# Optimization experiments

Hardware: AMD Instinct MI355X
Metric: run time of the kernel (lower is better)

Reference implementation:

```python
import jax, jax.numpy as jnp
import numpy as np

EPS = 1e-6

def _l2norm(t):
    # F.normalize over channel axis (axis=1) of (B, dk, L)
    n = jnp.sqrt(jnp.sum(t * t, axis=1, keepdims=True))
    return t / jnp.maximum(n, EPS)

def setup_inputs() -> dict:
    key = jax.random.key(0)
    ks = jax.random.split(key, 8)
    B, Cin, Cenc, dk, dv, H, W = 2, 64, 96, 64, 64, 96, 96
    return {
        "x": jax.random.normal(ks[0], (B, Cin, H, W), dtype=jnp.float32),
        "x_enc": jax.random.normal(ks[1], (B, Cenc, H, W), dtype=jnp.float32),
        "Wq": jax.random.normal(ks[2], (dk, Cenc), dtype=jnp.float32) * 0.05,
        "bq": jax.random.normal(ks[3], (dk,), dtype=jnp.float32) * 0.05,
        "Wk": jax.random.normal(ks[4], (dk, Cenc), dtype=jnp.float32) * 0.05,
        "bk": jax.random.normal(ks[5], (dk,), dtype=jnp.float32) * 0.05,
        "Wv": jax.random.normal(ks[6], (dv, Cin), dtype=jnp.float32) * 0.05,
        "bv": jax.random.normal(ks[7], (dv,), dtype=jnp.float32) * 0.05,
    }

def reference(x, x_enc, Wq, bq, Wk, bk, Wv, bv):
    B, _, H, W = x.shape
    L = H * W
    # 1x1 conv projections == channel matmuls, then flatten spatial dims
    Q = (jnp.einsum('bchw,kc->bkhw', x_enc, Wq) + bq[None, :, None, None]).reshape(B, -1, L)
    K = (jnp.einsum('bchw,kc->bkhw', x_enc, Wk) + bk[None, :, None, None]).reshape(B, -1, L)
    V = (jnp.einsum('bchw,kc->bkhw', x, Wv) + bv[None, :, None, None]).reshape(B, -1, L)
    # per-position L2 normalization over the dk channel axis ('l2' mode)
    Q = _l2norm(Q)
    K = _l2norm(K)
    # A[b,i,j] = sum_q Q[b,q,i] * K[b,q,j], softmax over j
    A = jax.nn.softmax(jnp.einsum('bqi,bqj->bij', Q, K), axis=-1)  # (B, L, L)
    R = jnp.einsum('bij,bvj->bvi', A, V)  # (B, dv, L)
    return R.reshape(B, -1, H, W)
```

## Files before the change

kernel.cpp:

```cpp
#include <hip/hip_runtime.h>
#include <hip/hip_bf16.h>
#include <math.h>

#define NB   2
#define CIN  64
#define CENC 96
#define DK   64
#define DV   64
#define LL   9216
#define QBLK 128
#define KVBLK 64
#define NQT  (LL/QBLK)
#define LOG2E 1.44269504088896340736f

typedef __attribute__((ext_vector_type(8)))  short short8;
typedef __attribute__((ext_vector_type(16))) float f32x16;
typedef __attribute__((ext_vector_type(2)))  unsigned int uint2v;
typedef unsigned int uint;

__device__ inline void gload16(const void* g, void* l) {
    __builtin_amdgcn_global_load_lds(
        (const __attribute__((address_space(1))) unsigned int*)g,
        (__attribute__((address_space(3))) unsigned int*)l, 16, 0, 0);
}

__device__ inline unsigned short f2bf(float f) {
    union { float f; uint u; } v; v.f = f;
    uint r = (v.u + 0x7FFFu + ((v.u >> 16) & 1u)) >> 16;
    return (unsigned short)r;
}

__device__ inline float bf2f(uint u) {
    union { uint u; float f; } c; c.u = u << 16; return c.f;
}

__device__ inline uint pack_bf16x2(float lo, float hi) {
    __hip_bfloat162 h = __float22bfloat162_rn(float2{lo, hi});
    union { __hip_bfloat162 h; uint u; } cvt; cvt.h = h;
    return cvt.u;
}

__device__ inline void plswap(uint& a, uint& b) {
#if __has_builtin(__builtin_amdgcn_permlane32_swap)
    uint2v r = __builtin_amdgcn_permlane32_swap(a, b, false, false);
    a = r.x; b = r.y;
#else
    const int lane = threadIdx.x & 63;
    uint t = (lane < 32) ? b : a;
    t = __shfl_xor(t, 32, 64);
    uint an = (lane < 32) ? a : t;
    uint bn = (lane < 32) ? t : b;
    a = an; b = bn;
#endif
}

__global__ __launch_bounds__(256) void proj_kernel(
    const float* __restrict__ x, const float* __restrict__ x_enc,
    const float* __restrict__ Wq, const float* __restrict__ bq,
    const float* __restrict__ Wk, const float* __restrict__ bk,
    const float* __restrict__ Wv, const float* __restrict__ bv,
    unsigned short* __restrict__ Qb, unsigned short* __restrict__ Kb,
    unsigned short* __restrict__ Vt, int nqk)
{
    __shared__ float sh[2 * CENC * 64];
    const int tid = threadIdx.x;

    if ((int)blockIdx.x < nqk) {
        float* Wt0 = sh;
        float* Wt1 = sh + CENC * 64;
        for (int idx = tid; idx < DK * CENC; idx += 256) {
            int k = idx / CENC, c = idx - k * CENC;
            Wt0[c * 64 + (k ^ (c & 31))] = Wq[idx];
            Wt1[c * 64 + (k ^ (c & 31))] = Wk[idx];
        }
        __syncthreads();

        const int w    = __builtin_amdgcn_readfirstlane(tid >> 6);
        const int lane = tid & 63;
        const int gw   = blockIdx.x * 4 + w;
        const int p0g  = gw * 16;
        const int b    = p0g / LL;
        const int p0   = p0g - b * LL;

        float qa[16], ka[16];
        const float bqv = bq[lane], bkv = bk[lane];
#pragma unroll
        for (int p = 0; p < 16; ++p) { qa[p] = bqv; ka[p] = bkv; }

        const float* xp = x_enc + (size_t)b * CENC * LL + p0;
#pragma unroll 4
        for (int c = 0; c < CENC; ++c) {
            const float wq = Wt0[c * 64 + (lane ^ (c & 31))];
            const float wk = Wt1[c * 64 + (lane ^ (c & 31))];
            const float* xc = xp + (size_t)c * LL;
#pragma unroll
            for (int p = 0; p < 16; ++p) {
                const float xv = xc[p];
                qa[p] = fmaf(wq, xv, qa[p]);
                ka[p] = fmaf(wk, xv, ka[p]);
            }
        }

        unsigned short* qrow = Qb + (size_t)(b * LL + p0) * 64 + lane;
        unsigned short* krow = Kb + (size_t)(b * LL + p0) * 64 + lane;
#pragma unroll
        for (int p = 0; p < 16; ++p) {
            float sq = qa[p] * qa[p];
            float sk = ka[p] * ka[p];
#pragma unroll
            for (int m = 1; m < 64; m <<= 1) {
                sq += __shfl_xor(sq, m, 64);
                sk += __shfl_xor(sk, m, 64);
            }
            qrow[(size_t)p * 64] = f2bf(qa[p] * (LOG2E / fmaxf(sqrtf(sq), 1e-6f)));
            krow[(size_t)p * 64] = f2bf(ka[p] * (1.f / fmaxf(sqrtf(sk), 1e-6f)));
        }
    } else {
        float* Wt = sh;
        unsigned short* Vsh = (unsigned short*)(sh + CIN * 64);
        for (int idx = tid; idx < DV * CIN; idx += 256) {
            int v = idx / CIN, c = idx - v * CIN;
            Wt[c * 64 + (v ^ (c & 31))] = Wv[idx];
        }
        __syncthreads();

        const int w    = __builtin_amdgcn_readfirstlane(tid >> 6);
        const int lane = tid & 63;
        const int l0g  = ((int)blockIdx.x - nqk) * 64;
        const int b    = l0g / LL;
        const int l0   = l0g - b * LL;
        const int p0   = w * 16;

        float va[16];
        const float bvv = bv[lane];
#pragma unroll
        for (int p = 0; p < 16; ++p) va[p] = bvv;

        const float* xp = x + (size_t)b * CIN * LL + l0 + p0;
#pragma unroll 4
        for (int c = 0; c < CIN; ++c) {
            const float wv = Wt[c * 64 + (lane ^ (c & 31))];
            const float* xc = xp + (size_t)c * LL;
#pragma unroll
            for (int p = 0; p < 16; ++p) va[p] = fmaf(wv, xc[p], va[p]);
        }
#pragma unroll
        for (int p = 0; p < 16; ++p) Vsh[(p0 + p) * 64 + lane] = f2bf(va[p]);
        __syncthreads();

        const int v = tid & 63, w2 = tid >> 6;
        uint pk[8];
#pragma unroll
        for (int j = 0; j < 8; ++j)
            pk[j] = (uint)Vsh[(w2 * 16 + 2 * j) * 64 + v] |
                    ((uint)Vsh[(w2 * 16 + 2 * j + 1) * 64 + v] << 16);
        uint4* dst = (uint4*)(Vt + (size_t)b * 64 * LL + (size_t)v * LL + l0 + w2 * 16);
        dst[0] = make_uint4(pk[0], pk[1], pk[2], pk[3]);
        dst[1] = make_uint4(pk[4], pk[5], pk[6], pk[7]);
    }
}

__global__ __launch_bounds__(256, 4) void flash_kernel(
    const unsigned short* __restrict__ Qb,
    const unsigned short* __restrict__ Kb,
    const unsigned short* __restrict__ Vt,
    float* __restrict__ Sp, unsigned short* __restrict__ Rp,
    int JS, int nt)
{
    __shared__ unsigned short Kl[2][KVBLK * 64];
    __shared__ unsigned short Vl[2][64 * KVBLK];

    const int bid0  = blockIdx.x;
    const int chunk = gridDim.x >> 3;
    const int bid   = (bid0 & 7) * chunk + (bid0 >> 3);

    const int qt  = bid % NQT;
    const int js  = (bid / NQT) % JS;
    const int b   = bid / (NQT * JS);
    const int tid = threadIdx.x;
    const int w = tid >> 6, lane = tid & 63;
    const int ln = lane & 31, h = lane >> 5;
    const int i0w = qt * QBLK + w * 32;

    short8 qf[4];
#pragma unroll
    for (int kc = 0; kc < 4; ++kc)
        qf[kc] = *(const short8*)(Qb + ((size_t)(b * LL + i0w + ln)) * 64 + kc * 16 + h * 8);

    const int o0 = w * 1024 + lane * 16;
    const int o1 = o0 + 4096;
    const int r0 = o0 >> 7, r1 = o1 >> 7;
    const int c0 = ((o0 >> 4) & 7) ^ (r0 & 7);
    const int c1 = ((o1 >> 4) & 7) ^ (r1 & 7);

    const unsigned short* KbB = Kb + (size_t)b * LL * 64;
    const unsigned short* VtB = Vt + (size_t)b * 64 * LL;

    f32x16 racc[2];
#pragma unroll
    for (int vg = 0; vg < 2; ++vg)
#pragma unroll
        for (int r = 0; r < 16; ++r) racc[vg][r] = 0.f;
    float ssum = 0.f;

    int j0 = js * nt * KVBLK;
    gload16(KbB + (size_t)(j0 + r0) * 64 + c0 * 8, (char*)Kl[0] + w * 1024);
    gload16(KbB + (size_t)(j0 + r1) * 64 + c1 * 8, (char*)Kl[0] + w * 1024 + 4096);
    gload16(VtB + (size_t)r0 * LL + j0 + c0 * 8, (char*)Vl[0] + w * 1024);
    gload16(VtB + (size_t)r1 * LL + j0 + c1 * 8, (char*)Vl[0] + w * 1024 + 4096);

    for (int t = 0; t < nt; ++t, j0 += KVBLK) {
        __syncthreads();
        const int bb = t & 1;
        if (t + 1 < nt) {
            const int j1 = j0 + KVBLK;
            gload16(KbB + (size_t)(j1 + r0) * 64 + c0 * 8, (char*)Kl[bb ^ 1] + w * 1024);
            gload16(KbB + (size_t)(j1 + r1) * 64 + c1 * 8, (char*)Kl[bb ^ 1] + w * 1024 + 4096);
            gload16(VtB + (size_t)r0 * LL + j1 + c0 * 8, (char*)Vl[bb ^ 1] + w * 1024);
            gload16(VtB + (size_t)r1 * LL + j1 + c1 * 8, (char*)Vl[bb ^ 1] + w * 1024 + 4096);
        }
        const char* Klb = (const char*)Kl[bb];
        const char* Vlb = (const char*)Vl[bb];

#pragma unroll
        for (int jt = 0; jt < 2; ++jt) {
            f32x16 sacc;
#pragma unroll
            for (int r = 0; r < 16; ++r) sacc[r] = 0.f;

            __builtin_amdgcn_s_setprio(1);
#pragma unroll
            for (int kc = 0; kc < 4; ++kc) {
                const int rowK = jt * 32 + ln;
                const short8 kf = *(const short8*)(Klb + rowK * 128 + (((kc << 1) + h) ^ (rowK & 7)) * 16);
                sacc = __builtin_amdgcn_mfma_f32_32x32x16_bf16(kf, qf[kc], sacc, 0, 0, 0);
            }
            __builtin_amdgcn_s_setprio(0);

#pragma unroll
            for (int r = 0; r < 16; ++r) sacc[r] = __builtin_amdgcn_exp2f(sacc[r]);
            float s0 = 0.f;
#pragma unroll
            for (int r = 0; r < 16; r += 4) s0 += (sacc[r] + sacc[r + 1]) + (sacc[r + 2] + sacc[r + 3]);
            ssum += s0;

            short8 pf[2];
            {
                uint u0[4], u1[4];
#pragma unroll
                for (int g = 0; g < 4; ++g) {
                    u0[g] = pack_bf16x2(sacc[4 * g], sacc[4 * g + 1]);
                    u1[g] = pack_bf16x2(sacc[4 * g + 2], sacc[4 * g + 3]);
                }
#pragma unroll
                for (int c = 0; c < 2; ++c) {
                    uint a0 = u0[2 * c], b0 = u0[2 * c + 1];
                    uint a1 = u1[2 * c], b1 = u1[2 * c + 1];
                    plswap(a0, b0);
                    plswap(a1, b1);
                    union { uint u[4]; short8 s; } P;
                    P.u[0] = a0; P.u[1] = a1; P.u[2] = b0; P.u[3] = b1;
                    pf[c] = P.s;
                }
            }

            __builtin_amdgcn_s_setprio(1);
#pragma unroll
            for (int c = 0; c < 2; ++c) {
                const int kcv = 2 * jt + c;
#pragma unroll
                for (int vg = 0; vg < 2; ++vg) {
                    const int rowV = vg * 32 + ln;
                    const short8 vf = *(const short8*)(Vlb + rowV * 128 + (((kcv << 1) + h) ^ (rowV & 7)) * 16);
                    racc[vg] = __builtin_amdgcn_mfma_f32_32x32x16_bf16(pf[c], vf, racc[vg], 0, 0, 0);
                }
            }
            __builtin_amdgcn_s_setprio(0);
        }
    }

    {
        float s = ssum + __shfl_xor(ssum, 32, 64);
        if (h == 0) Sp[(size_t)(b * JS + js) * LL + i0w + ln] = s;
    }

    __syncthreads();
    unsigned short* Tl = (unsigned short*)Kl;
#pragma unroll
    for (int vg = 0; vg < 2; ++vg) {
        const int v  = vg * 32 + ln;
        const int swz = (v & 7) << 4;
#pragma unroll
        for (int m = 0; m < 4; ++m) {
            uint2v u;
            u.x = pack_bf16x2(racc[vg][4 * m + 0], racc[vg][4 * m + 1]);
            u.y = pack_bf16x2(racc[vg][4 * m + 2], racc[vg][4 * m + 3]);
            const int byte = w * 64 + 8 * h + 16 * m;
            *(uint2v*)((char*)Tl + v * 256 + (byte ^ swz)) = u;
        }
    }
    __syncthreads();
    {
        const int v_loc = w * 16 + (lane >> 2);
        const int swzr  = (v_loc & 7) << 4;
        const char* rowp = (const char*)Tl + v_loc * 256;
        uint4 d[4];
#pragma unroll
        for (int k2 = 0; k2 < 4; ++k2)
            d[k2] = *(const uint4*)(rowp + ((((lane & 3) * 64) + k2 * 16) ^ swzr));
        const size_t rBase = (size_t)(b * JS + js) * 64;
        unsigned short* gdst = Rp + (rBase + v_loc) * (size_t)LL + qt * QBLK + (lane & 3) * 32;
#pragma unroll
        for (int k2 = 0; k2 < 4; ++k2)
            *(uint4*)(gdst + k2 * 8) = d[k2];
    }
}

__global__ __launch_bounds__(256) void combine_kernel(
    const float* __restrict__ Sp, const unsigned short* __restrict__ Rp,
    float* __restrict__ out, int JS)
{
    size_t g4 = ((size_t)blockIdx.x * 256 + threadIdx.x) * 4;
    int l = (int)(g4 % LL);
    int v = (int)((g4 / LL) % 64);
    int b = (int)(g4 / ((size_t)64 * LL));
    float4 s = make_float4(0.f, 0.f, 0.f, 0.f);
    float4 r = make_float4(0.f, 0.f, 0.f, 0.f);
    for (int js = 0; js < JS; ++js) {
        const float4 sv = *(const float4*)&Sp[(size_t)(b * JS + js) * LL + l];
        const uint2v rv = *(const uint2v*)&Rp[((size_t)(b * JS + js) * 64 + v) * LL + l];
        s.x += sv.x; s.y += sv.y; s.z += sv.z; s.w += sv.w;
        r.x += bf2f(rv.x & 0xffffu); r.y += bf2f(rv.x >> 16);
        r.z += bf2f(rv.y & 0xffffu); r.w += bf2f(rv.y >> 16);
    }
    *(float4*)&out[g4] = make_float4(r.x / s.x, r.y / s.y, r.z / s.z, r.w / s.w);
}

extern "C" void kernel_launch(void* const* d_in, const int* in_sizes, int n_in,
                              void* d_out, int out_size, void* d_ws, size_t ws_size,
                              hipStream_t stream) {
    (void)in_sizes; (void)n_in; (void)out_size;
    const float* x     = (const float*)d_in[0];
    const float* x_enc = (const float*)d_in[1];
    const float* Wq    = (const float*)d_in[2];
    const float* bq    = (const float*)d_in[3];
    const float* Wk    = (const float*)d_in[4];
    const float* bk    = (const float*)d_in[5];
    const float* Wv    = (const float*)d_in[6];
    const float* bv    = (const float*)d_in[7];
    float* out = (float*)d_out;
    char* ws = (char*)d_ws;

    const size_t nBF = (size_t)NB * LL * 64 * 2;
    unsigned short* Qb = (unsigned short*)ws;
    unsigned short* Kb = (unsigned short*)(ws + nBF);
    unsigned short* Vt = (unsigned short*)(ws + 2 * nBF);

    int JS = 8;
    {
        const int cand[3] = {16, 12, 8};
        for (int ci = 0; ci < 3; ++ci) {
            JS = cand[ci];
            size_t need = 3 * nBF + (size_t)NB * JS * LL * 4 + (size_t)NB * JS * 64 * LL * 2;
            if (need <= ws_size) break;
        }
    }
    float* Sp = (float*)(ws + 3 * nBF);
    unsigned short* Rp = (unsigned short*)(ws + 3 * nBF + (size_t)NB * JS * LL * 4);
    int nt = (LL / JS) / KVBLK;

    const int nqk = NB * LL / 64;
    proj_kernel   <<<2 * nqk, 256, 0, stream>>>(x, x_enc, Wq, bq, Wk, bk, Wv, bv, Qb, Kb, Vt, nqk);
    flash_kernel  <<<NB * JS * NQT, 256, 0, stream>>>(Qb, Kb, Vt, Sp, Rp, JS, nt);
    combine_kernel<<<(NB * 64 * LL) / 1024, 256, 0, stream>>>(Sp, Rp, out, JS);
}
```

Measured before the change: 116.6 us.

## Double query tile to 256 rows with 512-thread blocks sharing K/V tiles

Doubles the query block per workgroup (8 waves of 32 rows instead of 4) so each K/V tile staged in LDS is reused by twice as many query rows. Each thread now issues one async global-to-LDS load per K and V tile instead of two, and the shared buffer and output-transpose layout are widened to match. The grid halves, which lowers global K/V traffic but reduces the number of blocks and may affect occupancy with launch bounds of 512 threads x 4.

Result: no change. 116.0 us (-0.5%).

```diff
diff --git a/kernel.cpp b/kernel.cpp
--- a/kernel.cpp
+++ b/kernel.cpp
@@ -8,7 +8,7 @@
 #define DK   64
 #define DV   64
 #define LL   9216
-#define QBLK 128
+#define QBLK 256
 #define KVBLK 64
 #define NQT  (LL/QBLK)
 #define LOG2E 1.44269504088896340736f
@@ -160,15 +160,14 @@
     }
 }
 
-__global__ __launch_bounds__(256, 4) void flash_kernel(
+__global__ __launch_bounds__(512, 4) void flash_kernel(
     const unsigned short* __restrict__ Qb,
     const unsigned short* __restrict__ Kb,
     const unsigned short* __restrict__ Vt,
     float* __restrict__ Sp, unsigned short* __restrict__ Rp,
     int JS, int nt)
 {
-    __shared__ unsigned short Kl[2][KVBLK * 64];
-    __shared__ unsigned short Vl[2][64 * KVBLK];
+    __shared__ unsigned short Sh[16384];
 
     const int bid0  = blockIdx.x;
     const int chunk = gridDim.x >> 3;
@@ -188,10 +187,8 @@
         qf[kc] = *(const short8*)(Qb + ((size_t)(b * LL + i0w + ln)) * 64 + kc * 16 + h * 8);
 
     const int o0 = w * 1024 + lane * 16;
-    const int o1 = o0 + 4096;
-    const int r0 = o0 >> 7, r1 = o1 >> 7;
+    const int r0 = o0 >> 7;
     const int c0 = ((o0 >> 4) & 7) ^ (r0 & 7);
-    const int c1 = ((o1 >> 4) & 7) ^ (r1 & 7);
 
     const unsigned short* KbB = Kb + (size_t)b * LL * 64;
     const unsigned short* VtB = Vt + (size_t)b * 64 * LL;
@@ -204,23 +201,19 @@
     float ssum = 0.f;
 
     int j0 = js * nt * KVBLK;
-    gload16(KbB + (size_t)(j0 + r0) * 64 + c0 * 8, (char*)Kl[0] + w * 1024);
-    gload16(KbB + (size_t)(j0 + r1) * 64 + c1 * 8, (char*)Kl[0] + w * 1024 + 4096);
-    gload16(VtB + (size_t)r0 * LL + j0 + c0 * 8, (char*)Vl[0] + w * 1024);
-    gload16(VtB + (size_t)r1 * LL + j0 + c1 * 8, (char*)Vl[0] + w * 1024 + 4096);
+    gload16(KbB + (size_t)(j0 + r0) * 64 + c0 * 8, (char*)Sh + w * 1024);
+    gload16(VtB + (size_t)r0 * LL + j0 + c0 * 8, (char*)Sh + 16384 + w * 1024);
 
     for (int t = 0; t < nt; ++t, j0 += KVBLK) {
         __syncthreads();
         const int bb = t & 1;
         if (t + 1 < nt) {
             const int j1 = j0 + KVBLK;
-            gload16(KbB + (size_t)(j1 + r0) * 64 + c0 * 8, (char*)Kl[bb ^ 1] + w * 1024);
-            gload16(KbB + (size_t)(j1 + r1) * 64 + c1 * 8, (char*)Kl[bb ^ 1] + w * 1024 + 4096);
-            gload16(VtB + (size_t)r0 * LL + j1 + c0 * 8, (char*)Vl[bb ^ 1] + w * 1024);
-            gload16(VtB + (size_t)r1 * LL + j1 + c1 * 8, (char*)Vl[bb ^ 1] + w * 1024 + 4096);
-        }
-        const char* Klb = (const char*)Kl[bb];
-        const char* Vlb = (const char*)Vl[bb];
+            gload16(KbB + (size_t)(j1 + r0) * 64 + c0 * 8, (char*)Sh + (bb ^ 1) * 8192 + w * 1024);
+            gload16(VtB + (size_t)r0 * LL + j1 + c0 * 8, (char*)Sh + 16384 + (bb ^ 1) * 8192 + w * 1024);
+        }
+        const char* Klb = (const char*)Sh + bb * 8192;
+        const char* Vlb = (const char*)Sh + 16384 + bb * 8192;
 
 #pragma unroll
         for (int jt = 0; jt < 2; ++jt) {
@@ -246,16 +239,12 @@
 
             short8 pf[2];
             {
-                uint u0[4], u1[4];
-#pragma unroll
-                for (int g = 0; g < 4; ++g) {
-                    u0[g] = pack_bf16x2(sacc[4 * g], sacc[4 * g + 1]);
-                    u1[g] = pack_bf16x2(sacc[4 * g + 2], sacc[4 * g + 3]);
-                }
 #pragma unroll
                 for (int c = 0; c < 2; ++c) {
-                    uint a0 = u0[2 * c], b0 = u0[2 * c + 1];
-                    uint a1 = u1[2 * c], b1 = u1[2 * c + 1];
+                    uint a0 = pack_bf16x2(sacc[8 * c + 0], sacc[8 * c + 1]);
+                    uint b0 = pack_bf16x2(sacc[8 * c + 4], sacc[8 * c + 5]);
+                    uint a1 = pack_bf16x2(sacc[8 * c + 2], sacc[8 * c + 3]);
+                    uint b1 = pack_bf16x2(sacc[8 * c + 6], sacc[8 * c + 7]);
                     plswap(a0, b0);
                     plswap(a1, b1);
                     union { uint u[4]; short8 s; } P;
@@ -285,10 +274,10 @@
     }
 
     __syncthreads();
-    unsigned short* Tl = (unsigned short*)Kl;
+    unsigned short* Tl = Sh;
 #pragma unroll
     for (int vg = 0; vg < 2; ++vg) {
-        const int v  = vg * 32 + ln;
+        const int v   = vg * 32 + ln;
         const int swz = (v & 7) << 4;
 #pragma unroll
         for (int m = 0; m < 4; ++m) {
@@ -296,20 +285,20 @@
             u.x = pack_bf16x2(racc[vg][4 * m + 0], racc[vg][4 * m + 1]);
             u.y = pack_bf16x2(racc[vg][4 * m + 2], racc[vg][4 * m + 3]);
             const int byte = w * 64 + 8 * h + 16 * m;
-            *(uint2v*)((char*)Tl + v * 256 + (byte ^ swz)) = u;
+            *(uint2v*)((char*)Tl + v * 512 + (byte ^ swz)) = u;
         }
     }
     __syncthreads();
     {
-        const int v_loc = w * 16 + (lane >> 2);
+        const int v_loc = tid >> 3;
         const int swzr  = (v_loc & 7) << 4;
-        const char* rowp = (const char*)Tl + v_loc * 256;
+        const char* rowp = (const char*)Tl + v_loc * 512;
         uint4 d[4];
 #pragma unroll
         for (int k2 = 0; k2 < 4; ++k2)
-            d[k2] = *(const uint4*)(rowp + ((((lane & 3) * 64) + k2 * 16) ^ swzr));
+            d[k2] = *(const uint4*)(rowp + ((((tid & 7) * 64) + k2 * 16) ^ swzr));
         const size_t rBase = (size_t)(b * JS + js) * 64;
-        unsigned short* gdst = Rp + (rBase + v_loc) * (size_t)LL + qt * QBLK + (lane & 3) * 32;
+        unsigned short* gdst = Rp + (rBase + v_loc) * (size_t)LL + qt * QBLK + (tid & 7) * 32;
 #pragma unroll
         for (int k2 = 0; k2 < 4; ++k2)
             *(uint4*)(gdst + k2 * 8) = d[k2];
@@ -371,6 +360,6 @@
 
     const int nqk = NB * LL / 64;
     proj_kernel   <<<2 * nqk, 256, 0, stream>>>(x, x_enc, Wq, bq, Wk, bk, Wv, bv, Qb, Kb, Vt, nqk);
-    flash_kernel  <<<NB * JS * NQT, 256, 0, stream>>>(Qb, Kb, Vt, Sp, Rp, JS, nt);
+    flash_kernel  <<<NB * JS * NQT, 512, 0, stream>>>(Qb, Kb, Vt, Sp, Rp, JS, nt);
     combine_kernel<<<(NB * 64 * LL) / 1024, 256, 0, stream>>>(Sp, Rp, out, JS);
 }
```
